# Performance work log

Hardware: AMD Instinct MI355X
Metric: run time of the kernel (lower is better)

## Reference

```python
import jax, jax.numpy as jnp
import numpy as np

L, H, Wn, C = 2048, 768, 1024, 64


def setup_inputs() -> dict:
    key = jax.random.key(0)
    ks = jax.random.split(key, 12)
    s = 1.0 / np.sqrt(H)
    s3 = 1.0 / np.sqrt(3 * H)
    return {
        "tok_embs": jax.random.normal(ks[0], (L, H), jnp.float32),
        "wmask": jax.random.randint(ks[1], (L,), 0, Wn + 1),  # 1-indexed word positions, 0 = ignore
        "text_length": Wn,
        "label_embs": jax.random.normal(ks[2], (C, H), jnp.float32),
        "W_tok": jax.random.normal(ks[3], (H, 2 * H), jnp.float32) * s,
        "b_tok": jnp.zeros((2 * H,), jnp.float32),
        "W_lab": jax.random.normal(ks[4], (H, 2 * H), jnp.float32) * s,
        "b_lab": jnp.zeros((2 * H,), jnp.float32),
        "W1": jax.random.normal(ks[5], (3 * H, H), jnp.float32) * s3,
        "b1": jnp.zeros((H,), jnp.float32),
        "W2": jax.random.normal(ks[6], (H, 3), jnp.float32) * s,
        "b2": jnp.zeros((3,), jnp.float32),
    }


def reference(tok_embs, wmask, text_length, label_embs, W_tok, b_tok, W_lab, b_lab, W1, b1, W2, b2):
    Wd = text_length
    Hd = tok_embs.shape[-1]
    # --- word-level scatter pooling: we[wmask-1] = tok_embs where wmask > 0 ---
    # route masked-out tokens to a dummy row Wd, then drop it (jit-safe, no nonzero)
    tgt = jnp.where(wmask > 0, wmask - 1, Wd)
    we = jnp.zeros((Wd + 1, Hd), tok_embs.dtype).at[tgt].set(tok_embs)[:Wd]  # (W, H)
    # --- scorer ---
    t = (we @ W_tok + b_tok).reshape(Wd, 2, Hd)        # (W, 2, H)
    lb = (label_embs @ W_lab + b_lab).reshape(-1, 2, Hd)  # (C, 2, H)
    Cd = lb.shape[0]
    t0 = jnp.broadcast_to(t[:, None, 0, :], (Wd, Cd, Hd))
    l0 = jnp.broadcast_to(lb[None, :, 0, :], (Wd, Cd, Hd))
    prod = t[:, None, 1, :] * lb[None, :, 1, :]        # (W, C, H)
    cat = jnp.concatenate([t0, l0, prod], axis=-1)     # (W, C, 3H)
    h = jax.nn.relu(cat @ W1 + b1)                     # (W, C, H)
    scores = h @ W2 + b2                               # (W, C, 3)
    return scores
```

## Files before the change

### kernel.cpp

```cpp
#include <hip/hip_runtime.h>
#include <hip/hip_bf16.h>

static constexpr int Hd = 768;
static constexpr int H2 = 1536;
static constexpr int Cn = 64;

typedef __attribute__((ext_vector_type(8))) short short8;
typedef __attribute__((ext_vector_type(8))) _Float16 half8;
typedef __attribute__((ext_vector_type(4))) float f32x4;
typedef unsigned short us;

__device__ inline unsigned int f2bf2(float a, float b) {
    __hip_bfloat162 h = __float22bfloat162_rn(float2{a, b});
    return *reinterpret_cast<unsigned int*>(&h);
}

__device__ inline void split1(float x, us& h, us& l) {
    __hip_bfloat16 hb = __float2bfloat16(x);
    float hf = __bfloat162float(hb);
    __hip_bfloat16 lb_ = __float2bfloat16(x - hf);
    h = *reinterpret_cast<us*>(&hb);
    l = *reinterpret_cast<us*>(&lb_);
}

__device__ inline us f2b(float x) {
    __hip_bfloat16 b = __float2bfloat16(x);
    return *reinterpret_cast<us*>(&b);
}

__device__ inline us f2h(float x) {
    _Float16 h = (_Float16)x;
    return *reinterpret_cast<us*>(&h);
}

__device__ inline float b2f(us u) {
    __hip_bfloat16 b = *reinterpret_cast<__hip_bfloat16*>(&u);
    return __bfloat162float(b);
}

__device__ inline short8 hmul8(short8 a, short8 b) {
    half8 x = __builtin_bit_cast(half8, a);
    half8 y = __builtin_bit_cast(half8, b);
    half8 r = x * y;
    return __builtin_bit_cast(short8, r);
}

__device__ inline void gload16(const void* g, void* l) {
    __builtin_amdgcn_global_load_lds(
        (const __attribute__((address_space(1))) unsigned int*)g,
        (__attribute__((address_space(3))) unsigned int*)l, 16, 0, 0);
}

__global__ void k_init(int* widx, int Wd) {
    int i = blockIdx.x * 256 + threadIdx.x;
    if (i < Wd) widx[i] = -1;
}

__global__ void k_scatter(const int* __restrict__ wmask, int* widx, int L, int Wd) {
    int i = blockIdx.x * 256 + threadIdx.x;
    if (i < L) {
        int m = wmask[i];
        if (m > 0 && m <= Wd) atomicMax(&widx[m - 1], i);
    }
}

__global__ void k_build_we_split(const float4* __restrict__ tok, const int* __restrict__ widx,
                                 us* __restrict__ weh, us* __restrict__ wel, int Wd) {
    int i = blockIdx.x * 256 + threadIdx.x;
    if (i >= Wd * 192) return;
    int w = i / 192, c4 = i - w * 192;
    int idx = widx[w];
    float4 v = (idx >= 0) ? tok[idx * 192 + c4] : float4{0.f, 0.f, 0.f, 0.f};
    us hh[4], ll[4];
    split1(v.x, hh[0], ll[0]);
    split1(v.y, hh[1], ll[1]);
    split1(v.z, hh[2], ll[2]);
    split1(v.w, hh[3], ll[3]);
    size_t o = (size_t)w * Hd + c4 * 4;
    *(ushort4*)&weh[o] = ushort4{hh[0], hh[1], hh[2], hh[3]};
    *(ushort4*)&wel[o] = ushort4{ll[0], ll[1], ll[2], ll[3]};
}

struct TSArgs {
    const float* src[5];
    us* th[5];
    us* tl[5];
    int ld[5];
    int N[5];
    int fmt[5];
};
__global__ __launch_bounds__(256)
void k_tsplit(TSArgs a) {
    __shared__ float tile[64][65];
    const int z = blockIdx.z;
    const int n0 = blockIdx.x * 64, k0 = blockIdx.y * 64;
    if (n0 >= a.N[z]) return;
    const float* W = a.src[z];
    const int ld = a.ld[z];
    for (int idx = threadIdx.x; idx < 4096; idx += 256) {
        int kk = idx >> 6, nn = idx & 63;
        tile[kk][nn] = W[(size_t)(k0 + kk) * ld + n0 + nn];
    }
    __syncthreads();
    us* Th = a.th[z];
    us* Tl = a.tl[z];
    const int fmt = a.fmt[z];
    for (int idx = threadIdx.x; idx < 4096; idx += 256) {
        int nn = idx >> 6, kk = idx & 63;
        size_t o = (size_t)(n0 + nn) * Hd + k0 + kk;
        if (fmt) {
            Th[o] = f2h(tile[kk][nn]);
        } else {
            us h, l;
            split1(tile[kk][nn], h, l);
            Th[o] = h;
            Tl[o] = l;
        }
    }
}

__global__ __launch_bounds__(256)
void k_split(const float* __restrict__ x, int lda, int cols,
             us* __restrict__ h, us* __restrict__ l, int n4) {
    int i = blockIdx.x * 256 + threadIdx.x;
    if (i >= n4) return;
    int c4 = cols >> 2;
    int row = i / c4, cc = (i - row * c4) * 4;
    float4 v = *(const float4*)&x[(size_t)row * lda + cc];
    us hh[4], ll[4];
    split1(v.x, hh[0], ll[0]);
    split1(v.y, hh[1], ll[1]);
    split1(v.z, hh[2], ll[2]);
    split1(v.w, hh[3], ll[3]);
    size_t o = (size_t)row * cols + cc;
    *(ushort4*)&h[o] = ushort4{hh[0], hh[1], hh[2], hh[3]};
    *(ushort4*)&l[o] = ushort4{ll[0], ll[1], ll[2], ll[3]};
}

__global__ __launch_bounds__(256)
void k_gemm2(const us* __restrict__ Ah, const us* __restrict__ Al,
             const us* __restrict__ BhT, const us* __restrict__ BlT,
             float* __restrict__ Cpart, int M, int N, int K) {
    __shared__ __align__(16) us S[2][4][64 * 32];
    const int tid = threadIdx.x, wave = tid >> 6, lane = tid & 63;
    const int quad = lane >> 4, l15 = lane & 15;
    const int wm = wave & 1, wn = wave >> 1;
    const int m0 = blockIdx.y * 64, n0 = blockIdx.x * 64;
    const int Ks = K / gridDim.z, kbeg = blockIdx.z * Ks, kend = kbeg + Ks;
    float* C = Cpart + (size_t)blockIdx.z * M * N;

    const int srow = wave * 16 + (lane >> 2), soff = (lane & 3) * 8;
    const size_t gaB = (size_t)(m0 + srow) * K + soff;
    const size_t gbB = (size_t)(n0 + srow) * K + soff;
    const int lo = wave * 16 * 32;

    f32x4 acc[2][2];
#pragma unroll
    for (int a = 0; a < 2; ++a)
#pragma unroll
        for (int b = 0; b < 2; ++b) acc[a][b] = (f32x4){0.f, 0.f, 0.f, 0.f};

    auto stage = [&](int p, int k0) {
        gload16(Ah + gaB + k0, &S[p][0][lo]);
        gload16(Al + gaB + k0, &S[p][1][lo]);
        gload16(BhT + gbB + k0, &S[p][2][lo]);
        gload16(BlT + gbB + k0, &S[p][3][lo]);
    };

    int p = 0;
    stage(0, kbeg);
    for (int k0 = kbeg; k0 < kend; k0 += 32) {
        __syncthreads();
        if (k0 + 32 < kend) stage(p ^ 1, k0 + 32);
        short8 ah[2], al[2], bh[2], bl[2];
#pragma unroll
        for (int mt = 0; mt < 2; ++mt) {
            int off = (wm * 32 + mt * 16 + l15) * 32 + quad * 8;
            ah[mt] = *(const short8*)&S[p][0][off];
            al[mt] = *(const short8*)&S[p][1][off];
        }
#pragma unroll
        for (int nt = 0; nt < 2; ++nt) {
            int off = (wn * 32 + nt * 16 + l15) * 32 + quad * 8;
            bh[nt] = *(const short8*)&S[p][2][off];
            bl[nt] = *(const short8*)&S[p][3][off];
        }
#pragma unroll
        for (int mt = 0; mt < 2; ++mt)
#pragma unroll
            for (int nt = 0; nt < 2; ++nt) {
                acc[mt][nt] = __builtin_amdgcn_mfma_f32_16x16x32_bf16(al[mt], bh[nt], acc[mt][nt], 0, 0, 0);
                acc[mt][nt] = __builtin_amdgcn_mfma_f32_16x16x32_bf16(ah[mt], bl[nt], acc[mt][nt], 0, 0, 0);
                acc[mt][nt] = __builtin_amdgcn_mfma_f32_16x16x32_bf16(ah[mt], bh[nt], acc[mt][nt], 0, 0, 0);
            }
        p ^= 1;
    }
#pragma unroll
    for (int mt = 0; mt < 2; ++mt)
#pragma unroll
        for (int nt = 0; nt < 2; ++nt) {
            int col = n0 + wn * 32 + nt * 16 + l15;
#pragma unroll
            for (int reg = 0; reg < 4; ++reg) {
                int row = m0 + wm * 32 + mt * 16 + quad * 4 + reg;
                C[(size_t)row * N + col] = acc[mt][nt][reg];
            }
        }
}

__global__ __launch_bounds__(256)
void k_gemm3(const us* __restrict__ Ah, const us* __restrict__ Al,
             const us* __restrict__ BhT, const us* __restrict__ BlT,
             const float* __restrict__ bias, float* __restrict__ outF,
             us* __restrict__ sh, us* __restrict__ sl, us* __restrict__ bh16,
             int fp16out, int scols, int N, int K) {
    __shared__ __align__(16) us S[2][4][64 * 32];
    const int tid = threadIdx.x, wave = tid >> 6, lane = tid & 63;
    const int quad = lane >> 4, l15 = lane & 15;
    const int wm = wave & 1, wn = wave >> 1;
    const int m0 = blockIdx.y * 64, n0 = blockIdx.x * 64;

    const int srow = wave * 16 + (lane >> 2), soff = (lane & 3) * 8;
    const size_t gaB = (size_t)(m0 + srow) * K + soff;
    const size_t gbB = (size_t)(n0 + srow) * K + soff;
    const int lo = wave * 16 * 32;

    f32x4 acc[2][2];
#pragma unroll
    for (int a = 0; a < 2; ++a)
#pragma unroll
        for (int b = 0; b < 2; ++b) acc[a][b] = (f32x4){0.f, 0.f, 0.f, 0.f};

    auto stage = [&](int p, int k0) {
        gload16(Ah + gaB + k0, &S[p][0][lo]);
        gload16(Al + gaB + k0, &S[p][1][lo]);
        gload16(BhT + gbB + k0, &S[p][2][lo]);
        gload16(BlT + gbB + k0, &S[p][3][lo]);
    };

    int p = 0;
    stage(0, 0);
    for (int k0 = 0; k0 < K; k0 += 32) {
        __syncthreads();
        if (k0 + 32 < K) stage(p ^ 1, k0 + 32);
        short8 ah[2], al[2], bh[2], bl[2];
#pragma unroll
        for (int mt = 0; mt < 2; ++mt) {
            int off = (wm * 32 + mt * 16 + l15) * 32 + quad * 8;
            ah[mt] = *(const short8*)&S[p][0][off];
            al[mt] = *(const short8*)&S[p][1][off];
        }
#pragma unroll
        for (int nt = 0; nt < 2; ++nt) {
            int off = (wn * 32 + nt * 16 + l15) * 32 + quad * 8;
            bh[nt] = *(const short8*)&S[p][2][off];
            bl[nt] = *(const short8*)&S[p][3][off];
        }
#pragma unroll
        for (int mt = 0; mt < 2; ++mt)
#pragma unroll
            for (int nt = 0; nt < 2; ++nt) {
                acc[mt][nt] = __builtin_amdgcn_mfma_f32_16x16x32_bf16(al[mt], bh[nt], acc[mt][nt], 0, 0, 0);
                acc[mt][nt] = __builtin_amdgcn_mfma_f32_16x16x32_bf16(ah[mt], bl[nt], acc[mt][nt], 0, 0, 0);
                acc[mt][nt] = __builtin_amdgcn_mfma_f32_16x16x32_bf16(ah[mt], bh[nt], acc[mt][nt], 0, 0, 0);
            }
        p ^= 1;
    }
#pragma unroll
    for (int mt = 0; mt < 2; ++mt)
#pragma unroll
        for (int nt = 0; nt < 2; ++nt) {
            int col = n0 + wn * 32 + nt * 16 + l15;
            float bb = bias ? bias[col] : 0.f;
#pragma unroll
            for (int reg = 0; reg < 4; ++reg) {
                int row = m0 + wm * 32 + mt * 16 + quad * 4 + reg;
                float v = acc[mt][nt][reg] + bb;
                if (outF) outF[(size_t)row * N + col] = v;
                if (sh) {
                    if (col < scols) {
                        us h, l;
                        split1(v, h, l);
                        size_t o = (size_t)row * scols + col;
                        sh[o] = h;
                        sl[o] = l;
                    } else if (bh16) {
                        bh16[(size_t)row * scols + (col - scols)] = fp16out ? f2h(v) : f2b(v);
                    }
                }
            }
        }
}

__global__ __launch_bounds__(256)
void k_reduce(const float* __restrict__ part, int S, int MN, int N,
              const float* __restrict__ bias, float* __restrict__ outF,
              us* __restrict__ sh, us* __restrict__ sl, int scols,
              us* __restrict__ bh16, int fp16out) {
    int i = blockIdx.x * 256 + threadIdx.x;
    if (i >= MN) return;
    float v = 0.f;
    for (int s = 0; s < S; ++s) v += part[(size_t)s * MN + i];
    int row = i / N, col = i - row * N;
    if (bias) v += bias[col];
    if (outF) outF[i] = v;
    if (col < scols) {
        if (sh) {
            us h, l;
            split1(v, h, l);
            size_t o = (size_t)row * scols + col;
            sh[o] = h;
            sl[o] = l;
        }
    } else if (bh16) {
        bh16[(size_t)row * scols + (col - scols)] = fp16out ? f2h(v) : f2b(v);
    }
}

__global__ __launch_bounds__(256, 2)
void k_mfma8(const us* __restrict__ t1b,
             const us* __restrict__ W1ct,
             const us* __restrict__ lb1b,
             const float* __restrict__ Aw,
             const float* __restrict__ Bc,
             const float* __restrict__ W2,
             float* __restrict__ scr) {
    __shared__ __align__(16) us As[2][4096];
    __shared__ __align__(16) us Bs[2][4096];
    __shared__ __align__(16) us lbs[2][Hd];
    __shared__ float sred[2 * 128 * 3];

    const int tid = threadIdx.x, wave = tid >> 6, lane = tid & 63;
    const int quad = lane >> 4, l15 = lane & 15;
    const int wm = wave & 1, wn = wave >> 1;

    const int b = blockIdx.x;
    const int xcd = b & 7, slot = b >> 3;
    const int jx = slot >> 5;
    const int cp = slot & 31;
    const int c0 = cp * 2;
    const int jt = jx * 128, m0 = xcd * 128;

    for (int i = tid; i < 2 * 128 * 3; i += 256) sred[i] = 0.f;
    if (tid < 192) {
        int cc = tid / 96, o = (tid - cc * 96) * 8;
        *(short8*)&lbs[cc][o] = *(const short8*)&lb1b[(size_t)(c0 + cc) * Hd + o];
    }

    const int srow = (wave & 1) * 64 + lane;
    const int skq = (wave >> 1) * 8;
    const us* gA = W1ct + (size_t)(jt + srow) * Hd + skq;
    const us* gB = t1b + (size_t)(m0 + srow) * Hd + skq;

    f32x4 acc0[4][4], acc1[4][4];
#pragma unroll
    for (int mt = 0; mt < 4; ++mt)
#pragma unroll
        for (int nt = 0; nt < 4; ++nt) {
            acc0[mt][nt] = (f32x4){0.f, 0.f, 0.f, 0.f};
            acc1[mt][nt] = (f32x4){0.f, 0.f, 0.f, 0.f};
        }

    auto stage = [&](int p, int k0) {
        gload16(gA + k0,      &As[p][wave * 512]);
        gload16(gA + k0 + 16, &As[p][(wave + 4) * 512]);
        gload16(gB + k0,      &Bs[p][wave * 512]);
        gload16(gB + k0 + 16, &Bs[p][(wave + 4) * 512]);
    };

    const int rbA = quad * 1024 + (wm * 64 + l15) * 8;
    const int rbB = quad * 1024 + (wn * 64 + l15) * 8;

    stage(0, 0);
    int p = 0;
    for (int k0 = 0; k0 < Hd; k0 += 32) {
        __syncthreads();
        if (k0 + 32 < Hd) stage(p ^ 1, k0 + 32);
        short8 af[4], bf[4];
#pragma unroll
        for (int mt = 0; mt < 4; ++mt) af[mt] = *(const short8*)&As[p][rbA + mt * 128];
#pragma unroll
        for (int nt = 0; nt < 4; ++nt) bf[nt] = *(const short8*)&Bs[p][rbB + nt * 128];
        short8 lv0 = *(const short8*)&lbs[0][k0 + quad * 8];
        short8 lv1 = *(const short8*)&lbs[1][k0 + quad * 8];
#pragma unroll
        for (int mt = 0; mt < 4; ++mt) {
            short8 a0 = hmul8(af[mt], lv0);
            short8 a1 = hmul8(af[mt], lv1);
#pragma unroll
            for (int nt = 0; nt < 4; ++nt) {
                acc0[mt][nt] = __builtin_amdgcn_mfma_f32_16x16x32_f16(
                    __builtin_bit_cast(half8, a0),
                    __builtin_bit_cast(half8, bf[nt]), acc0[mt][nt], 0, 0, 0);
                acc1[mt][nt] = __builtin_amdgcn_mfma_f32_16x16x32_f16(
                    __builtin_bit_cast(half8, a1),
                    __builtin_bit_cast(half8, bf[nt]), acc1[mt][nt], 0, 0, 0);
            }
        }
        p ^= 1;
    }

    float bcv0[4][4], bcv1[4][4], w2v[4][4][3];
#pragma unroll
    for (int mt = 0; mt < 4; ++mt) {
        const int jb = jt + wm * 64 + mt * 16 + quad * 4;
        float4 b4 = *(const float4*)&Bc[(size_t)c0 * Hd + jb];
        bcv0[mt][0] = b4.x; bcv0[mt][1] = b4.y; bcv0[mt][2] = b4.z; bcv0[mt][3] = b4.w;
        float4 b5 = *(const float4*)&Bc[(size_t)(c0 + 1) * Hd + jb];
        bcv1[mt][0] = b5.x; bcv1[mt][1] = b5.y; bcv1[mt][2] = b5.z; bcv1[mt][3] = b5.w;
#pragma unroll
        for (int reg = 0; reg < 4; ++reg)
#pragma unroll
            for (int r = 0; r < 3; ++r) w2v[mt][reg][r] = W2[(jb + reg) * 3 + r];
    }

    auto reduce_c = [&](const f32x4 (&ac)[4][4], const float (&bcv)[4][4], int cc) {
#pragma unroll
        for (int nt = 0; nt < 4; ++nt) {
            const int w = m0 + wn * 64 + nt * 16 + l15;
            const float* awp = Aw + (size_t)w * Hd + jt + wm * 64;
            float s0 = 0.f, s1 = 0.f, s2 = 0.f;
#pragma unroll
            for (int mt = 0; mt < 4; ++mt) {
                float4 a4 = *(const float4*)&awp[mt * 16 + quad * 4];
                float av[4] = {a4.x, a4.y, a4.z, a4.w};
#pragma unroll
                for (int reg = 0; reg < 4; ++reg) {
                    float h = ac[mt][nt][reg] + av[reg] + bcv[mt][reg];
                    h = h > 0.f ? h : 0.f;
                    s0 += h * w2v[mt][reg][0];
                    s1 += h * w2v[mt][reg][1];
                    s2 += h * w2v[mt][reg][2];
                }
            }
            s0 += __shfl_xor(s0, 16); s0 += __shfl_xor(s0, 32);
            s1 += __shfl_xor(s1, 16); s1 += __shfl_xor(s1, 32);
            s2 += __shfl_xor(s2, 16); s2 += __shfl_xor(s2, 32);
            if (quad == 0) {
                const int wl = wn * 64 + nt * 16 + l15;
                atomicAdd(&sred[cc * 384 + wl * 3 + 0], s0);
                atomicAdd(&sred[cc * 384 + wl * 3 + 1], s1);
                atomicAdd(&sred[cc * 384 + wl * 3 + 2], s2);
            }
        }
    };
    reduce_c(acc0, bcv0, 0);
    reduce_c(acc1, bcv1, 1);
    __syncthreads();

    float* slab = scr + ((size_t)jx * 1024 * Cn + (size_t)m0 * Cn) * 3;
    for (int i = tid; i < 2 * 128 * 3; i += 256) {
        int cc = i / 384, j = i - cc * 384;
        int wl = j / 3, r = j - wl * 3;
        slab[((size_t)wl * Cn + (c0 + cc)) * 3 + r] = sred[i];
    }
}

__global__ __launch_bounds__(256)
void k_scores(const float* __restrict__ scr, const float* __restrict__ b2,
              float* __restrict__ out, int n) {
    int i = blockIdx.x * 256 + threadIdx.x;
    if (i >= n) return;
    float v = b2[i % 3];
#pragma unroll
    for (int s = 0; s < 6; ++s) v += scr[(size_t)s * n + i];
    out[i] = v;
}

extern "C" void kernel_launch(void* const* d_in, const int* in_sizes, int n_in,
                              void* d_out, int out_size, void* d_ws, size_t ws_size,
                              hipStream_t stream) {
    const float* tok    = (const float*)d_in[0];
    const int*   wmask  = (const int*)d_in[1];
    const float* labe   = (const float*)d_in[3];
    const float* W_tok  = (const float*)d_in[4];
    const float* b_tok  = (const float*)d_in[5];
    const float* W_lab  = (const float*)d_in[6];
    const float* b_lab  = (const float*)d_in[7];
    const float* W1     = (const float*)d_in[8];
    const float* b1     = (const float*)d_in[9];
    const float* W2     = (const float*)d_in[10];
    const float* b2     = (const float*)d_in[11];
    float* out = (float*)d_out;

    const int L  = in_sizes[1];
    const int Wd = out_size / (Cn * 3);

    char* ws = (char*)d_ws;
    size_t off = 0;
    auto alloc = [&](size_t bytes) { char* p = ws + off; off += (bytes + 255) & ~(size_t)255; return p; };
    int*   widx  = (int*)alloc(4096);
    float* Abuf  = (float*)alloc((size_t)Wd * Hd * 4);
    float* Bbuf  = (float*)alloc((size_t)Cn * Hd * 4);
    us* W1ct  = (us*)alloc((size_t)Hd * Hd * 2);
    us* W1cl  = (us*)alloc((size_t)Hd * Hd * 2);
    us* t1b   = (us*)alloc((size_t)Wd * Hd * 2);
    us* lb1b  = (us*)alloc((size_t)Cn * Hd * 2);
    float* scr = (float*)alloc((size_t)6 * Wd * Cn * 3 * 4);
    us* WtTh  = (us*)alloc((size_t)H2 * Hd * 2);
    us* WtTl  = (us*)alloc((size_t)H2 * Hd * 2);
    us* WlTh  = (us*)alloc((size_t)H2 * Hd * 2);
    us* WlTl  = (us*)alloc((size_t)H2 * Hd * 2);
    us* W1aTh = (us*)alloc((size_t)Hd * Hd * 2);
    us* W1aTl = (us*)alloc((size_t)Hd * Hd * 2);
    us* W1bTh = (us*)alloc((size_t)Hd * Hd * 2);
    us* W1bTl = (us*)alloc((size_t)Hd * Hd * 2);
    us* weh   = (us*)alloc((size_t)Wd * Hd * 2);
    us* wel   = (us*)alloc((size_t)Wd * Hd * 2);
    us* lah   = (us*)alloc((size_t)Cn * Hd * 2);
    us* lal   = (us*)alloc((size_t)Cn * Hd * 2);
    us* t0h   = (us*)alloc((size_t)Wd * Hd * 2);
    us* t0l   = (us*)alloc((size_t)Wd * Hd * 2);
    us* lb0h  = (us*)alloc((size_t)Cn * Hd * 2);
    us* lb0l  = (us*)alloc((size_t)Cn * Hd * 2);
    float* part = (float*)alloc((size_t)8 * Cn * H2 * 4);

    k_init<<<(Wd + 255) / 256, 256, 0, stream>>>(widx, Wd);
    k_scatter<<<(L + 255) / 256, 256, 0, stream>>>(wmask, widx, L, Wd);
    k_build_we_split<<<(Wd * 192 + 255) / 256, 256, 0, stream>>>((const float4*)tok, widx, weh, wel, Wd);

    TSArgs ts;
    ts.src[0] = W_tok;  ts.th[0] = WtTh;  ts.tl[0] = WtTl;  ts.ld[0] = H2; ts.N[0] = H2; ts.fmt[0] = 0;
    ts.src[1] = W_lab;  ts.th[1] = WlTh;  ts.tl[1] = WlTl;  ts.ld[1] = H2; ts.N[1] = H2; ts.fmt[1] = 0;
    ts.src[2] = W1;                         ts.th[2] = W1aTh; ts.tl[2] = W1aTl; ts.ld[2] = Hd; ts.N[2] = Hd; ts.fmt[2] = 0;
    ts.src[3] = W1 + (size_t)Hd * Hd;       ts.th[3] = W1bTh; ts.tl[3] = W1bTl; ts.ld[3] = Hd; ts.N[3] = Hd; ts.fmt[3] = 0;
    ts.src[4] = W1 + (size_t)2 * Hd * Hd;   ts.th[4] = W1ct;  ts.tl[4] = W1cl;  ts.ld[4] = Hd; ts.N[4] = Hd; ts.fmt[4] = 1;
    k_tsplit<<<dim3(H2 / 64, Hd / 64, 5), 256, 0, stream>>>(ts);

    k_split<<<(Cn * Hd / 4 + 255) / 256, 256, 0, stream>>>(labe, Hd, Hd, lah, lal, Cn * Hd / 4);

    k_gemm3<<<dim3(H2 / 64, Wd / 64), 256, 0, stream>>>(weh, wel, WtTh, WtTl, b_tok,
                                                        nullptr, t0h, t0l, t1b, 1, Hd, H2, Hd);

    k_gemm2<<<dim3(H2 / 64, 1, 8), 256, 0, stream>>>(lah, lal, WlTh, WlTl, part, Cn, H2, Hd);
    k_reduce<<<(Cn * H2 + 255) / 256, 256, 0, stream>>>(part, 8, Cn * H2, H2, b_lab, nullptr, lb0h, lb0l, Hd, lb1b, 1);

    k_gemm3<<<dim3(Hd / 64, Wd / 64), 256, 0, stream>>>(t0h, t0l, W1aTh, W1aTl, nullptr,
                                                        Abuf, nullptr, nullptr, nullptr, 0, 0, Hd, Hd);

    k_gemm2<<<dim3(Hd / 64, 1, 8), 256, 0, stream>>>(lb0h, lb0l, W1bTh, W1bTl, part, Cn, Hd, Hd);
    k_reduce<<<(Cn * Hd + 255) / 256, 256, 0, stream>>>(part, 8, Cn * Hd, Hd, b1, Bbuf, nullptr, nullptr, Hd, nullptr, 0);

    k_mfma8<<<1536, 256, 0, stream>>>(t1b, W1ct, lb1b, Abuf, Bbuf, W2, scr);

    k_scores<<<(Wd * Cn * 3 + 255) / 256, 256, 0, stream>>>(scr, b2, out, Wd * Cn * 3);
}
```

Before: 257.8 us.

## Retile main MFMA kernel to 256x256 tiles, one label, triple-buffered LDS

Replaces the 128x128, two-label, 256-thread MFMA kernel with a 512-thread kernel. Each block computes a 256(j) x 256(w) tile for a single label over the full K, using a 3-stage global_load_lds pipeline with explicit waitcnt, split-phase staging, and setprio around the MFMA bursts. This raises arithmetic intensity per LDS load and halves the number of partial-score slabs (6 to 3) that k_scores reduces. In exchange each block holds more accumulators, occupancy drops to one block per CU, and the hand-placed barriers make the code more fragile.

```diff
diff --git a/kernel.cpp b/kernel.cpp
--- a/kernel.cpp
+++ b/kernel.cpp
@@ -9,11 +9,6 @@
 typedef __attribute__((ext_vector_type(8))) _Float16 half8;
 typedef __attribute__((ext_vector_type(4))) float f32x4;
 typedef unsigned short us;
-
-__device__ inline unsigned int f2bf2(float a, float b) {
-    __hip_bfloat162 h = __float22bfloat162_rn(float2{a, b});
-    return *reinterpret_cast<unsigned int*>(&h);
-}
 
 __device__ inline void split1(float x, us& h, us& l) {
     __hip_bfloat16 hb = __float2bfloat16(x);
@@ -31,11 +26,6 @@
 __device__ inline us f2h(float x) {
     _Float16 h = (_Float16)x;
     return *reinterpret_cast<us*>(&h);
-}
-
-__device__ inline float b2f(us u) {
-    __hip_bfloat16 b = *reinterpret_cast<__hip_bfloat16*>(&u);
-    return __bfloat162float(b);
 }
 
 __device__ inline short8 hmul8(short8 a, short8 b) {
@@ -317,142 +307,158 @@
     }
 }
 
-__global__ __launch_bounds__(256, 2)
-void k_mfma8(const us* __restrict__ t1b,
-             const us* __restrict__ W1ct,
-             const us* __restrict__ lb1b,
-             const float* __restrict__ Aw,
-             const float* __restrict__ Bc,
-             const float* __restrict__ W2,
-             float* __restrict__ scr) {
-    __shared__ __align__(16) us As[2][4096];
-    __shared__ __align__(16) us Bs[2][4096];
-    __shared__ __align__(16) us lbs[2][Hd];
-    __shared__ float sred[2 * 128 * 3];
+__global__ __launch_bounds__(512, 1)
+void k_mfma13(const us* __restrict__ t1b,
+              const us* __restrict__ W1ct,
+              const us* __restrict__ lb1b,
+              const float* __restrict__ Aw,
+              const float* __restrict__ Bc,
+              const float* __restrict__ W2,
+              float* __restrict__ scr) {
+    __shared__ __align__(16) us RA[3][8192];
+    __shared__ __align__(16) us RB[3][8192];
+    __shared__ __align__(16) us lbs[Hd];
+    __shared__ float sred[256 * 3];
 
     const int tid = threadIdx.x, wave = tid >> 6, lane = tid & 63;
     const int quad = lane >> 4, l15 = lane & 15;
-    const int wm = wave & 1, wn = wave >> 1;
+    const int wm2 = wave >> 2, wn4 = wave & 3;
 
     const int b = blockIdx.x;
-    const int xcd = b & 7, slot = b >> 3;
-    const int jx = slot >> 5;
-    const int cp = slot & 31;
-    const int c0 = cp * 2;
-    const int jt = jx * 128, m0 = xcd * 128;
-
-    for (int i = tid; i < 2 * 128 * 3; i += 256) sred[i] = 0.f;
-    if (tid < 192) {
-        int cc = tid / 96, o = (tid - cc * 96) * 8;
-        *(short8*)&lbs[cc][o] = *(const short8*)&lb1b[(size_t)(c0 + cc) * Hd + o];
-    }
-
-    const int srow = (wave & 1) * 64 + lane;
-    const int skq = (wave >> 1) * 8;
-    const us* gA = W1ct + (size_t)(jt + srow) * Hd + skq;
-    const us* gB = t1b + (size_t)(m0 + srow) * Hd + skq;
-
-    f32x4 acc0[4][4], acc1[4][4];
-#pragma unroll
-    for (int mt = 0; mt < 4; ++mt)
-#pragma unroll
-        for (int nt = 0; nt < 4; ++nt) {
-            acc0[mt][nt] = (f32x4){0.f, 0.f, 0.f, 0.f};
-            acc1[mt][nt] = (f32x4){0.f, 0.f, 0.f, 0.f};
-        }
-
-    auto stage = [&](int p, int k0) {
-        gload16(gA + k0,      &As[p][wave * 512]);
-        gload16(gA + k0 + 16, &As[p][(wave + 4) * 512]);
-        gload16(gB + k0,      &Bs[p][wave * 512]);
-        gload16(gB + k0 + 16, &Bs[p][(wave + 4) * 512]);
+    const int xcd = b & 7, s5 = b >> 3;
+    const int cl = s5 & 7, idx = s5 >> 3;
+    const int jb = idx % 3, wb = idx / 3;
+    const int c  = xcd * 8 + cl;
+
+    for (int i = tid; i < 256 * 3; i += 512) sred[i] = 0.f;
+    if (tid < 96) *(short8*)&lbs[tid * 8] = *(const short8*)&lb1b[(size_t)c * Hd + tid * 8];
+
+    const int q = wave & 3, rh = wave >> 2;
+    const us* gA0 = W1ct + (size_t)(jb * 256 + (rh * 2 + 0) * 64 + lane) * Hd + q * 8;
+    const us* gA1 = W1ct + (size_t)(jb * 256 + (rh * 2 + 1) * 64 + lane) * Hd + q * 8;
+    const us* gB0 = t1b + (size_t)(wb * 256 + (rh * 2 + 0) * 64 + lane) * Hd + q * 8;
+    const us* gB1 = t1b + (size_t)(wb * 256 + (rh * 2 + 1) * 64 + lane) * Hd + q * 8;
+    const int dA0 = q * 2048 + (rh * 2 + 0) * 512;
+    const int dA1 = q * 2048 + (rh * 2 + 1) * 512;
+
+    f32x4 acc[8][4];
+#pragma unroll
+    for (int mf = 0; mf < 8; ++mf)
+#pragma unroll
+        for (int nf = 0; nf < 4; ++nf) acc[mf][nf] = (f32x4){0.f, 0.f, 0.f, 0.f};
+
+    auto stagePh = [&](int slot, int k0, int j) {
+        if (j == 0) { gload16(gA0 + k0, &RA[slot][dA0]); gload16(gB0 + k0, &RB[slot][dA0]); }
+        else        { gload16(gA1 + k0, &RA[slot][dA1]); gload16(gB1 + k0, &RB[slot][dA1]); }
     };
 
-    const int rbA = quad * 1024 + (wm * 64 + l15) * 8;
-    const int rbB = quad * 1024 + (wn * 64 + l15) * 8;
-
-    stage(0, 0);
-    int p = 0;
-    for (int k0 = 0; k0 < Hd; k0 += 32) {
-        __syncthreads();
-        if (k0 + 32 < Hd) stage(p ^ 1, k0 + 32);
-        short8 af[4], bf[4];
-#pragma unroll
-        for (int mt = 0; mt < 4; ++mt) af[mt] = *(const short8*)&As[p][rbA + mt * 128];
-#pragma unroll
-        for (int nt = 0; nt < 4; ++nt) bf[nt] = *(const short8*)&Bs[p][rbB + nt * 128];
-        short8 lv0 = *(const short8*)&lbs[0][k0 + quad * 8];
-        short8 lv1 = *(const short8*)&lbs[1][k0 + quad * 8];
-#pragma unroll
-        for (int mt = 0; mt < 4; ++mt) {
-            short8 a0 = hmul8(af[mt], lv0);
-            short8 a1 = hmul8(af[mt], lv1);
-#pragma unroll
-            for (int nt = 0; nt < 4; ++nt) {
-                acc0[mt][nt] = __builtin_amdgcn_mfma_f32_16x16x32_f16(
-                    __builtin_bit_cast(half8, a0),
-                    __builtin_bit_cast(half8, bf[nt]), acc0[mt][nt], 0, 0, 0);
-                acc1[mt][nt] = __builtin_amdgcn_mfma_f32_16x16x32_f16(
-                    __builtin_bit_cast(half8, a1),
-                    __builtin_bit_cast(half8, bf[nt]), acc1[mt][nt], 0, 0, 0);
+    const int rbA = quad * 2048 + (wm2 * 128 + l15) * 8;
+    const int rbB = quad * 2048 + (wn4 * 64 + l15) * 8;
+
+    __syncthreads();
+
+    stagePh(0, 0, 0);  stagePh(0, 0, 1);
+    stagePh(1, 32, 0); stagePh(1, 32, 1);
+
+#pragma unroll
+    for (int s = 0; s < 24; ++s) {
+        const int slot = s % 3;
+        if (s < 23) asm volatile("s_waitcnt vmcnt(4)" ::: "memory");
+        else        asm volatile("s_waitcnt vmcnt(0)" ::: "memory");
+        __builtin_amdgcn_s_barrier();
+        __builtin_amdgcn_sched_barrier(0);
+        short8 bF[4], aF[4];
+        short8 lv = *(const short8*)&lbs[s * 32 + quad * 8];
+#pragma unroll
+        for (int nf = 0; nf < 4; ++nf) bF[nf] = *(const short8*)&RB[slot][rbB + nf * 128];
+#pragma unroll
+        for (int i = 0; i < 4; ++i) aF[i] = *(const short8*)&RA[slot][rbA + i * 128];
+        if (s + 2 < 24) stagePh((s + 2) % 3, (s + 2) * 32, 0);
+        asm volatile("s_waitcnt lgkmcnt(0)" ::: "memory");
+        __builtin_amdgcn_sched_barrier(0);
+        __builtin_amdgcn_s_setprio(1);
+#pragma unroll
+        for (int i = 0; i < 4; ++i) {
+            short8 aS = hmul8(aF[i], lv);
+#pragma unroll
+            for (int nf = 0; nf < 4; ++nf)
+                acc[i][nf] = __builtin_amdgcn_mfma_f32_16x16x32_f16(
+                    __builtin_bit_cast(half8, aS),
+                    __builtin_bit_cast(half8, bF[nf]), acc[i][nf], 0, 0, 0);
+        }
+        __builtin_amdgcn_s_setprio(0);
+        __builtin_amdgcn_s_barrier();
+#pragma unroll
+        for (int i = 0; i < 4; ++i) aF[i] = *(const short8*)&RA[slot][rbA + (4 + i) * 128];
+        if (s + 2 < 24) stagePh((s + 2) % 3, (s + 2) * 32, 1);
+        asm volatile("s_waitcnt lgkmcnt(0)" ::: "memory");
+        __builtin_amdgcn_sched_barrier(0);
+        __builtin_amdgcn_s_setprio(1);
+#pragma unroll
+        for (int i = 0; i < 4; ++i) {
+            short8 aS = hmul8(aF[i], lv);
+#pragma unroll
+            for (int nf = 0; nf < 4; ++nf)
+                acc[4 + i][nf] = __builtin_amdgcn_mfma_f32_16x16x32_f16(
+                    __builtin_bit_cast(half8, aS),
+                    __builtin_bit_cast(half8, bF[nf]), acc[4 + i][nf], 0, 0, 0);
+        }
+        __builtin_amdgcn_s_setprio(0);
+    }
+
+    float sv[4][3];
+#pragma unroll
+    for (int nf = 0; nf < 4; ++nf)
+#pragma unroll
+        for (int r = 0; r < 3; ++r) sv[nf][r] = 0.f;
+
+#pragma unroll
+    for (int mf = 0; mf < 8; ++mf) {
+        const int jg = jb * 256 + wm2 * 128 + mf * 16 + quad * 4;
+        float4 bc4 = *(const float4*)&Bc[(size_t)c * Hd + jg];
+        float bcv[4] = {bc4.x, bc4.y, bc4.z, bc4.w};
+        float w2v[4][3];
+#pragma unroll
+        for (int reg = 0; reg < 4; ++reg)
+#pragma unroll
+            for (int r = 0; r < 3; ++r) w2v[reg][r] = W2[(jg + reg) * 3 + r];
+#pragma unroll
+        for (int nf = 0; nf < 4; ++nf) {
+            const int w = wb * 256 + wn4 * 64 + nf * 16 + l15;
+            float4 a4 = *(const float4*)&Aw[(size_t)w * Hd + jg];
+            float av[4] = {a4.x, a4.y, a4.z, a4.w};
+#pragma unroll
+            for (int reg = 0; reg < 4; ++reg) {
+                float h = acc[mf][nf][reg] + av[reg] + bcv[reg];
+                h = h > 0.f ? h : 0.f;
+                sv[nf][0] += h * w2v[reg][0];
+                sv[nf][1] += h * w2v[reg][1];
+                sv[nf][2] += h * w2v[reg][2];
             }
         }
-        p ^= 1;
-    }
-
-    float bcv0[4][4], bcv1[4][4], w2v[4][4][3];
-#pragma unroll
-    for (int mt = 0; mt < 4; ++mt) {
-        const int jb = jt + wm * 64 + mt * 16 + quad * 4;
-        float4 b4 = *(const float4*)&Bc[(size_t)c0 * Hd + jb];
-        bcv0[mt][0] = b4.x; bcv0[mt][1] = b4.y; bcv0[mt][2] = b4.z; bcv0[mt][3] = b4.w;
-        float4 b5 = *(const float4*)&Bc[(size_t)(c0 + 1) * Hd + jb];
-        bcv1[mt][0] = b5.x; bcv1[mt][1] = b5.y; bcv1[mt][2] = b5.z; bcv1[mt][3] = b5.w;
-#pragma unroll
-        for (int reg = 0; reg < 4; ++reg)
-#pragma unroll
-            for (int r = 0; r < 3; ++r) w2v[mt][reg][r] = W2[(jb + reg) * 3 + r];
-    }
-
-    auto reduce_c = [&](const f32x4 (&ac)[4][4], const float (&bcv)[4][4], int cc) {
-#pragma unroll
-        for (int nt = 0; nt < 4; ++nt) {
-            const int w = m0 + wn * 64 + nt * 16 + l15;
-            const float* awp = Aw + (size_t)w * Hd + jt + wm * 64;
-            float s0 = 0.f, s1 = 0.f, s2 = 0.f;
-#pragma unroll
-            for (int mt = 0; mt < 4; ++mt) {
-                float4 a4 = *(const float4*)&awp[mt * 16 + quad * 4];
-                float av[4] = {a4.x, a4.y, a4.z, a4.w};
-#pragma unroll
-                for (int reg = 0; reg < 4; ++reg) {
-                    float h = ac[mt][nt][reg] + av[reg] + bcv[mt][reg];
-                    h = h > 0.f ? h : 0.f;
-                    s0 += h * w2v[mt][reg][0];
-                    s1 += h * w2v[mt][reg][1];
-                    s2 += h * w2v[mt][reg][2];
-                }
-            }
-            s0 += __shfl_xor(s0, 16); s0 += __shfl_xor(s0, 32);
-            s1 += __shfl_xor(s1, 16); s1 += __shfl_xor(s1, 32);
-            s2 += __shfl_xor(s2, 16); s2 += __shfl_xor(s2, 32);
-            if (quad == 0) {
-                const int wl = wn * 64 + nt * 16 + l15;
-                atomicAdd(&sred[cc * 384 + wl * 3 + 0], s0);
-                atomicAdd(&sred[cc * 384 + wl * 3 + 1], s1);
-                atomicAdd(&sred[cc * 384 + wl * 3 + 2], s2);
-            }
-        }
-    };
-    reduce_c(acc0, bcv0, 0);
-    reduce_c(acc1, bcv1, 1);
+    }
+#pragma unroll
+    for (int nf = 0; nf < 4; ++nf) {
+#pragma unroll
+        for (int r = 0; r < 3; ++r) {
+            float s = sv[nf][r];
+            s += __shfl_xor(s, 16);
+            s += __shfl_xor(s, 32);
+            sv[nf][r] = s;
+        }
+        if (quad == 0) {
+            const int wl = wn4 * 64 + nf * 16 + l15;
+            atomicAdd(&sred[wl * 3 + 0], sv[nf][0]);
+            atomicAdd(&sred[wl * 3 + 1], sv[nf][1]);
+            atomicAdd(&sred[wl * 3 + 2], sv[nf][2]);
+        }
+    }
     __syncthreads();
 
-    float* slab = scr + ((size_t)jx * 1024 * Cn + (size_t)m0 * Cn) * 3;
-    for (int i = tid; i < 2 * 128 * 3; i += 256) {
-        int cc = i / 384, j = i - cc * 384;
-        int wl = j / 3, r = j - wl * 3;
-        slab[((size_t)wl * Cn + (c0 + cc)) * 3 + r] = sred[i];
+    float* slab = scr + (size_t)jb * (1024 * Cn * 3);
+    for (int i = tid; i < 256 * 3; i += 512) {
+        int wl = i / 3, r = i - wl * 3;
+        slab[((size_t)(wb * 256 + wl) * Cn + c) * 3 + r] = sred[i];
     }
 }
 
@@ -463,7 +469,7 @@
     if (i >= n) return;
     float v = b2[i % 3];
 #pragma unroll
-    for (int s = 0; s < 6; ++s) v += scr[(size_t)s * n + i];
+    for (int s = 0; s < 3; ++s) v += scr[(size_t)s * n + i];
     out[i] = v;
 }
 
@@ -496,7 +502,7 @@
     us* W1cl  = (us*)alloc((size_t)Hd * Hd * 2);
     us* t1b   = (us*)alloc((size_t)Wd * Hd * 2);
     us* lb1b  = (us*)alloc((size_t)Cn * Hd * 2);
-    float* scr = (float*)alloc((size_t)6 * Wd * Cn * 3 * 4);
+    float* scr = (float*)alloc((size_t)3 * Wd * Cn * 3 * 4);
     us* WtTh  = (us*)alloc((size_t)H2 * Hd * 2);
     us* WtTl  = (us*)alloc((size_t)H2 * Hd * 2);
     us* WlTh  = (us*)alloc((size_t)H2 * Hd * 2);
@@ -541,7 +547,7 @@
     k_gemm2<<<dim3(Hd / 64, 1, 8), 256, 0, stream>>>(lb0h, lb0l, W1bTh, W1bTl, part, Cn, Hd, Hd);
     k_reduce<<<(Cn * Hd + 255) / 256, 256, 0, stream>>>(part, 8, Cn * Hd, Hd, b1, Bbuf, nullptr, nullptr, Hd, nullptr, 0);
 
-    k_mfma8<<<1536, 256, 0, stream>>>(t1b, W1ct, lb1b, Abuf, Bbuf, W2, scr);
+    k_mfma13<<<768, 512, 0, stream>>>(t1b, W1ct, lb1b, Abuf, Bbuf, W2, scr);
 
     k_scores<<<(Wd * Cn * 3 + 255) / 256, 256, 0, stream>>>(scr, b2, out, Wd * Cn * 3);
 }
```

Result: slower. 308.8 us (+19.8%).
